# Kernel tuning notes

Measured on AMD Instinct MI355X. Metric: run time of the kernel, lower is better.

Reference implementation:

```python
import jax, jax.numpy as jnp
import numpy as np

NUM_HEADS = 12


def setup_inputs() -> dict:
    key = jax.random.key(0)
    ks = jax.random.split(key, 7)
    B, H, W, C = 1, 64, 64, 768
    hd = C // NUM_HEADS
    return {
        "x": jax.random.normal(ks[0], (B, H, W, C), dtype=jnp.float32),
        "qkv_w": jax.random.normal(ks[1], (C, 3 * C), dtype=jnp.float32) * 0.02,
        "qkv_b": jax.random.normal(ks[2], (3 * C,), dtype=jnp.float32) * 0.02,
        "proj_w": jax.random.normal(ks[3], (C, C), dtype=jnp.float32) * 0.02,
        "proj_b": jax.random.normal(ks[4], (C,), dtype=jnp.float32) * 0.02,
        "rel_pos_h": jax.random.normal(ks[5], (2 * H - 1, hd), dtype=jnp.float32) * 0.02,
        "rel_pos_w": jax.random.normal(ks[6], (2 * W - 1, hd), dtype=jnp.float32) * 0.02,
    }


def _rel_table(size, rel_pos):
    # q_size == k_size so relative_coords = i - j + (size - 1)
    coords = jnp.arange(size)[:, None] - jnp.arange(size)[None, :] + (size - 1)
    return rel_pos[coords]  # [size, size, head_dim]


def reference(x, qkv_w, qkv_b, proj_w, proj_b, rel_pos_h, rel_pos_w):
    B, H, W, C = x.shape
    nh = NUM_HEADS
    hd = C // nh
    scale = hd ** -0.5
    N = H * W

    qkv = x.reshape(B, N, C) @ qkv_w + qkv_b  # [B, N, 3C]
    qkv = qkv.reshape(B, N, 3, nh, hd).transpose(2, 0, 3, 1, 4).reshape(3, B * nh, N, hd)
    q, k, v = qkv[0], qkv[1], qkv[2]

    attn = jnp.einsum("bqd,bkd->bqk", q * scale, k)  # [B*nh, N, N]

    # decomposed relative position bias
    Rh = _rel_table(H, rel_pos_h)  # [H, H, hd]
    Rw = _rel_table(W, rel_pos_w)  # [W, W, hd]
    qr = q.reshape(B * nh, H, W, hd)
    rel_h = jnp.einsum("bhwc,hkc->bhwk", qr, Rh)  # [B*nh, H, W, H]
    rel_w = jnp.einsum("bhwc,wkc->bhwk", qr, Rw)  # [B*nh, H, W, W]
    bias = rel_h[..., :, None] + rel_w[..., None, :]  # [B*nh, H, W, H, W]
    attn = attn + bias.reshape(B * nh, N, N)

    attn = jax.nn.softmax(attn, axis=-1)
    out = jnp.einsum("bqk,bkd->bqd", attn, v)  # [B*nh, N, hd]
    out = out.reshape(B, nh, H, W, hd).transpose(0, 2, 3, 1, 4).reshape(B, H, W, C)
    return out @ proj_w + proj_b
```

## Files before the change

kernel.cpp:

```cpp
#include <hip/hip_runtime.h>
#include <math.h>

#define NHEADS 12
#define NTOK 4096
#define LOG2E 1.44269504f

typedef __attribute__((ext_vector_type(8))) short bf8v;
typedef __attribute__((ext_vector_type(4))) float f4v;
typedef __attribute__((ext_vector_type(16))) float f16v;

__device__ __forceinline__ unsigned short f2bf(float f) {
  unsigned int u = __float_as_uint(f);
  u += 0x7fffu + ((u >> 16) & 1u);
  return (unsigned short)(u >> 16);
}
__device__ __forceinline__ bf8v pack8(float4 a, float4 b) {
  bf8v v;
  v[0] = (short)f2bf(a.x); v[1] = (short)f2bf(a.y);
  v[2] = (short)f2bf(a.z); v[3] = (short)f2bf(a.w);
  v[4] = (short)f2bf(b.x); v[5] = (short)f2bf(b.y);
  v[6] = (short)f2bf(b.z); v[7] = (short)f2bf(b.w);
  return v;
}
__device__ __forceinline__ unsigned pkbf(float hi, float lo) {
  return __builtin_amdgcn_perm(__float_as_uint(hi) + 0x8000u,
                               __float_as_uint(lo) + 0x8000u, 0x07060302u);
}
__device__ __forceinline__ void gload_lds16(const void* g, void* l) {
  __builtin_amdgcn_global_load_lds(
      (const __attribute__((address_space(1))) void*)g,
      (__attribute__((address_space(3))) void*)l, 16, 0, 0);
}

__device__ __forceinline__ void tcvt_body(
    const float* __restrict__ in, short* __restrict__ out, int R, int C,
    int bx, int by, int t, float (*Ts)[65])
{
    const int bc = bx * 64, br = by * 64;
    {
        const int r = t >> 2, c0 = (t & 3) * 16;
        const float* src = in + (size_t)(br + r) * C + bc + c0;
#pragma unroll
        for (int i = 0; i < 4; ++i) {
            float4 a = *(const float4*)(src + 4 * i);
            Ts[r][c0 + 4 * i + 0] = a.x;
            Ts[r][c0 + 4 * i + 1] = a.y;
            Ts[r][c0 + 4 * i + 2] = a.z;
            Ts[r][c0 + 4 * i + 3] = a.w;
        }
    }
    __syncthreads();
    const int c = t >> 2, r0 = (t & 3) * 16;
    short* dst = out + (size_t)(bc + c) * R + br + r0;
#pragma unroll
    for (int p = 0; p < 2; ++p) {
        bf8v v;
#pragma unroll
        for (int i = 0; i < 8; ++i) v[i] = (short)f2bf(Ts[r0 + p * 8 + i][c]);
        *(bf8v*)(dst + p * 8) = v;
    }
}

__global__ __launch_bounds__(256) void prep_kernel(
    const float* __restrict__ x, const float* __restrict__ qkvw,
    const float* __restrict__ pw, short* __restrict__ xh,
    short* __restrict__ wqkvT, short* __restrict__ pwT)
{
    __shared__ float Ts[64][65];
    const int bid = blockIdx.x, t = threadIdx.x;
    if (bid < 1536) {
        const size_t i = ((size_t)bid * 256 + t) * 8;
        float4 a = *(const float4*)(x + i);
        float4 b = *(const float4*)(x + i + 4);
        *(bf8v*)(xh + i) = pack8(a, b);
    } else if (bid < 1968) {
        const int idx = bid - 1536;
        tcvt_body(qkvw, wqkvT, 768, 2304, idx % 36, idx / 36, t, Ts);
    } else {
        const int idx = bid - 1968;
        tcvt_body(pw, pwT, 768, 768, idx % 12, idx / 12, t, Ts);
    }
}

__global__ __launch_bounds__(256) void qkv_mfma_kernel(
    const short* __restrict__ xh, const short* __restrict__ wT,
    const float* __restrict__ bias, short* __restrict__ qbh,
    short* __restrict__ kbh, short* __restrict__ vbT)
{
    __shared__ __align__(16) short As[128 * 32];
    __shared__ __align__(16) short Bs[96 * 32];
    const int t = threadIdx.x;
    const int w = t >> 6, lane = t & 63;
    const int l15 = lane & 15, l4 = lane >> 4;
    const int wr = w >> 1, wc = w & 1;
    const int row0 = blockIdx.y * 128, col0 = blockIdx.x * 96;
    const int ldr = lane >> 2;
    const int ldk = (lane & 3) * 8;

    f4v acc[4][3] = {};
    const short* aBase = xh + (size_t)(row0 + w * 32 + ldr) * 768 + ldk;
    const short* bBase0 = wT + (size_t)(col0 + w * 16 + ldr) * 768 + ldk;
    const short* bBase1 = wT + (size_t)(col0 + 64 + w * 16 + ldr) * 768 + ldk;

    for (int kk = 0; kk < 768; kk += 32) {
        __syncthreads();
#pragma unroll
        for (int c = 0; c < 2; ++c)
            gload_lds16(aBase + (size_t)c * 16 * 768 + kk,
                        &As[(w * 32 + c * 16) * 32]);
        gload_lds16(bBase0 + kk, &Bs[(w * 16) * 32]);
        if (w < 2)
            gload_lds16(bBase1 + kk, &Bs[(64 + w * 16) * 32]);
        __syncthreads();
        bf8v af[4], bg[3];
#pragma unroll
        for (int i = 0; i < 4; ++i)
            af[i] = *(const bf8v*)&As[(wr * 64 + 16 * i + l15) * 32 + l4 * 8];
#pragma unroll
        for (int j = 0; j < 3; ++j)
            bg[j] = *(const bf8v*)&Bs[(wc * 48 + 16 * j + l15) * 32 + l4 * 8];
#pragma unroll
        for (int i = 0; i < 4; ++i)
#pragma unroll
            for (int j = 0; j < 3; ++j)
                acc[i][j] = __builtin_amdgcn_mfma_f32_16x16x32_bf16(
                    af[i], bg[j], acc[i][j], 0, 0, 0);
    }

#pragma unroll
    for (int j = 0; j < 3; ++j) {
        const int n = col0 + wc * 48 + 16 * j + l15;
        const int s = n / 768;
        const int rm = n - s * 768;
        const int h = rm >> 6, d = rm & 63;
        const float bv = bias[n];
        if (s == 2) {
            short* vdst = vbT + (size_t)(h * 64 + d) * NTOK;
#pragma unroll
            for (int i = 0; i < 4; ++i) {
                const int m = row0 + wr * 64 + 16 * i + l4 * 4;
                short4 pv;
                pv.x = (short)f2bf(acc[i][j][0] + bv);
                pv.y = (short)f2bf(acc[i][j][1] + bv);
                pv.z = (short)f2bf(acc[i][j][2] + bv);
                pv.w = (short)f2bf(acc[i][j][3] + bv);
                *(short4*)(vdst + m) = pv;
            }
        } else {
            short* dst = (s == 0) ? qbh : kbh;
#pragma unroll
            for (int i = 0; i < 4; ++i) {
                const int m = row0 + wr * 64 + 16 * i + l4 * 4;
#pragma unroll
                for (int r = 0; r < 4; ++r)
                    dst[((size_t)h * NTOK + m + r) * 64 + d] =
                        (short)f2bf(acc[i][j][r] + bv);
            }
        }
    }
}

union FlashSMem {
    struct {
        short Ks[128][68];
        short Vt[64][132];
        float relHs[64][65];
    };
    float U[128 * 65];
    struct {
        float OEp[64][64];
        float lEp[64];
    };
};

__global__ __launch_bounds__(256, 3) void flash_mfma_kernel(
    const short* __restrict__ qbh, const short* __restrict__ kbh,
    const short* __restrict__ vbT, const float* __restrict__ rpw,
    const float* __restrict__ rph, short* __restrict__ aob)
{
    __shared__ __align__(16) FlashSMem sm;

    const int t = threadIdx.x;
    const int qt = blockIdx.x, head = blockIdx.y;
    const int row0 = qt * 64;
    const int lane = t & 63, w = t >> 6;
    const int qh2 = w & 1, th = w >> 1;
    const int l31 = lane & 31, hf = lane >> 5;
    const size_t hB = (size_t)head * NTOK * 64;
    const float SC = 0.125f * LOG2E;

    const int q = row0 + qh2 * 32 + l31;
    bf8v bQ[4];
    {
        const short* qsrc = qbh + hB + (size_t)q * 64;
#pragma unroll
        for (int ks = 0; ks < 4; ++ks)
            bQ[ks] = *(const bf8v*)(qsrc + ks * 16 + hf * 8);
    }
    const int sx = t >> 2;
    const int sck = (t & 3) * 16;
    const int scv = (t & 3) * 32;
    const short* kptr = kbh + hB + (size_t)sx * 64 + sck;
    const short* vptr = vbT + ((size_t)head * 64 + sx) * NTOK + scv;
    bf8v kpf[4], vpf[4];
    kpf[0] = *(const bf8v*)(kptr);
    kpf[1] = *(const bf8v*)(kptr + 8);
    kpf[2] = *(const bf8v*)(kptr + 64 * 64);
    kpf[3] = *(const bf8v*)(kptr + 64 * 64 + 8);
    vpf[0] = *(const bf8v*)(vptr);
    vpf[1] = *(const bf8v*)(vptr + 8);
    vpf[2] = *(const bf8v*)(vptr + 16);
    vpf[3] = *(const bf8v*)(vptr + 24);

#pragma unroll
    for (int jt2 = 0; jt2 < 2; ++jt2) {
        const int jt = 2 * th + jt2;
        int j = jt * 32 + l31;
        if (j > 126) j = 0;
        const float* asrc = rpw + (size_t)j * 64;
        f16v c = {};
#pragma unroll
        for (int ks = 0; ks < 4; ++ks) {
            float4 u0 = *(const float4*)(asrc + ks * 16 + hf * 8);
            float4 u1 = *(const float4*)(asrc + ks * 16 + hf * 8 + 4);
            c = __builtin_amdgcn_mfma_f32_32x32x16_bf16(
                pack8(u0, u1), bQ[ks], c, 0, 0, 0);
        }
#pragma unroll
        for (int reg = 0; reg < 16; ++reg)
            sm.U[(jt * 32 + (reg & 3) + 8 * (reg >> 2) + 4 * hf) * 65 +
                 qh2 * 32 + l31] = c[reg];
    }
    __syncthreads();
    const int qw = qh2 * 32 + l31;
    uint2 rwp[2][4];
#pragma unroll
    for (int t32 = 0; t32 < 2; ++t32)
#pragma unroll
        for (int g = 0; g < 4; ++g) {
            const int kw = t32 * 32 + 8 * g + 4 * hf;
            const float v0 = sm.U[(qw + 63 - kw) * 65 + qw] * LOG2E;
            const float v1 = sm.U[(qw + 62 - kw) * 65 + qw] * LOG2E;
            const float v2 = sm.U[(qw + 61 - kw) * 65 + qw] * LOG2E;
            const float v3 = sm.U[(qw + 60 - kw) * 65 + qw] * LOG2E;
            rwp[t32][g].x = pkbf(v1, v0);
            rwp[t32][g].y = pkbf(v3, v2);
        }
    __syncthreads();

    {
        const int kh = th * 32 + l31;
        const float* asrc = rph + (size_t)(qt + 63 - kh) * 64;
        f16v c = {};
#pragma unroll
        for (int ks = 0; ks < 4; ++ks) {
            float4 u0 = *(const float4*)(asrc + ks * 16 + hf * 8);
            float4 u1 = *(const float4*)(asrc + ks * 16 + hf * 8 + 4);
            u0.x *= LOG2E; u0.y *= LOG2E; u0.z *= LOG2E; u0.w *= LOG2E;
            u1.x *= LOG2E; u1.y *= LOG2E; u1.z *= LOG2E; u1.w *= LOG2E;
            c = __builtin_amdgcn_mfma_f32_32x32x16_bf16(
                pack8(u0, u1), bQ[ks], c, 0, 0, 0);
        }
#pragma unroll
        for (int reg = 0; reg < 16; ++reg)
            sm.relHs[th * 32 + (reg & 3) + 8 * (reg >> 2) + 4 * hf]
                    [qh2 * 32 + l31] = c[reg];
    }

    f16v O[2] = {{}, {}};
    float lsum = 0.f;

    for (int it = 0; it < 32; ++it) {
        __syncthreads();
        *(bf8v*)&sm.Ks[sx][sck] = kpf[0];
        *(bf8v*)&sm.Ks[sx][sck + 8] = kpf[1];
        *(bf8v*)&sm.Ks[sx + 64][sck] = kpf[2];
        *(bf8v*)&sm.Ks[sx + 64][sck + 8] = kpf[3];
        *(bf8v*)&sm.Vt[sx][scv] = vpf[0];
        *(bf8v*)&sm.Vt[sx][scv + 8] = vpf[1];
        *(bf8v*)&sm.Vt[sx][scv + 16] = vpf[2];
        *(bf8v*)&sm.Vt[sx][scv + 24] = vpf[3];
        {
            const int itn = (it < 31) ? it + 1 : 31;
            const short* kp = kptr + (size_t)itn * 128 * 64;
            const short* vp = vptr + itn * 128;
            kpf[0] = *(const bf8v*)kp;
            kpf[1] = *(const bf8v*)(kp + 8);
            kpf[2] = *(const bf8v*)(kp + 64 * 64);
            kpf[3] = *(const bf8v*)(kp + 64 * 64 + 8);
            vpf[0] = *(const bf8v*)vp;
            vpf[1] = *(const bf8v*)(vp + 8);
            vpf[2] = *(const bf8v*)(vp + 16);
            vpf[3] = *(const bf8v*)(vp + 24);
        }
        __syncthreads();

        f16v acc[2] = {{}, {}};
#pragma unroll
        for (int ks = 0; ks < 4; ++ks)
#pragma unroll
            for (int t32 = 0; t32 < 2; ++t32)
                acc[t32] = __builtin_amdgcn_mfma_f32_32x32x16_bf16(
                    *(const bf8v*)&sm.Ks[th * 64 + t32 * 32 + l31]
                                        [ks * 16 + hf * 8],
                    bQ[ks], acc[t32], 0, 0, 0);

        const float rh = sm.relHs[2 * it + th][qh2 * 32 + l31];

        unsigned xg[2][4], yg[2][4];
#pragma unroll
        for (int t32 = 0; t32 < 2; ++t32) {
            float sub = 0.f;
#pragma unroll
            for (int g = 0; g < 4; ++g) {
                const unsigned u0 = rwp[t32][g].x;
                const unsigned u1 = rwp[t32][g].y;
                const float b0 = __uint_as_float(u0 << 16) + rh;
                const float b1 = __uint_as_float(u0 & 0xffff0000u) + rh;
                const float b2 = __uint_as_float(u1 << 16) + rh;
                const float b3 = __uint_as_float(u1 & 0xffff0000u) + rh;
                const float e0 = __builtin_amdgcn_exp2f(
                    fmaf(acc[t32][4 * g + 0], SC, b0));
                const float e1 = __builtin_amdgcn_exp2f(
                    fmaf(acc[t32][4 * g + 1], SC, b1));
                const float e2 = __builtin_amdgcn_exp2f(
                    fmaf(acc[t32][4 * g + 2], SC, b2));
                const float e3 = __builtin_amdgcn_exp2f(
                    fmaf(acc[t32][4 * g + 3], SC, b3));
                sub += (e0 + e1) + (e2 + e3);
                xg[t32][g] = pkbf(e1, e0);
                yg[t32][g] = pkbf(e3, e2);
            }
            lsum += sub;
        }

#pragma unroll
        for (int t32 = 0; t32 < 2; ++t32)
#pragma unroll
            for (int ks2 = 0; ks2 < 2; ++ks2) {
                auto px = __builtin_amdgcn_permlane32_swap(
                    xg[t32][2 * ks2], xg[t32][2 * ks2 + 1], false, false);
                auto py = __builtin_amdgcn_permlane32_swap(
                    yg[t32][2 * ks2], yg[t32][2 * ks2 + 1], false, false);
                int4 av;
                av.x = (int)px[0];
                av.y = (int)py[0];
                av.z = (int)px[1];
                av.w = (int)py[1];
                union { int4 i; bf8v v; } u; u.i = av;
#pragma unroll
                for (int nt = 0; nt < 2; ++nt)
                    O[nt] = __builtin_amdgcn_mfma_f32_32x32x16_bf16(
                        u.v,
                        *(const bf8v*)&sm.Vt[nt * 32 + l31]
                                            [th * 64 + t32 * 32 + ks2 * 16 +
                                             hf * 8],
                        O[nt], 0, 0, 0);
            }
    }

    lsum += __shfl_xor(lsum, 32);
    __syncthreads();
    if (th == 1) {
#pragma unroll
        for (int nt = 0; nt < 2; ++nt)
#pragma unroll
            for (int reg = 0; reg < 16; ++reg) {
                const int qr = (reg & 3) + 8 * (reg >> 2) + 4 * hf;
                sm.OEp[qh2 * 32 + qr][nt * 32 + l31] = O[nt][reg];
            }
        if (lane < 32) sm.lEp[qh2 * 32 + l31] = lsum;
    }
    __syncthreads();
    if (th == 0) {
        lsum += sm.lEp[qh2 * 32 + l31];
        const float linv = 1.0f / lsum;
#pragma unroll
        for (int nt = 0; nt < 2; ++nt)
#pragma unroll
            for (int reg = 0; reg < 16; ++reg) {
                const int qr = (reg & 3) + 8 * (reg >> 2) + 4 * hf;
                const float li = __shfl(linv, qr);
                const float o =
                    O[nt][reg] + sm.OEp[qh2 * 32 + qr][nt * 32 + l31];
                aob[(size_t)(row0 + qh2 * 32 + qr) * 768 + head * 64 +
                    nt * 32 + l31] = (short)f2bf(o * li);
            }
    }
}

__global__ __launch_bounds__(256) void proj_mfma_kernel(
    const short* __restrict__ aoh, const short* __restrict__ pwT,
    const float* __restrict__ bias, float* __restrict__ out)
{
    __shared__ __align__(16) short As[64 * 32];
    __shared__ __align__(16) short Bs[128 * 32];
    const int t = threadIdx.x;
    const int w = t >> 6, lane = t & 63;
    const int l15 = lane & 15, l4 = lane >> 4;
    const int wr = w >> 1, wc = w & 1;
    const int row0 = blockIdx.y * 64, col0 = blockIdx.x * 128;
    const int ldr = lane >> 2;
    const int ldk = (lane & 3) * 8;

    f4v acc[2][4] = {};
    const short* aBase = aoh + (size_t)(row0 + w * 16 + ldr) * 768 + ldk;
    const short* bBase = pwT + (size_t)(col0 + w * 32 + ldr) * 768 + ldk;

    for (int kk = 0; kk < 768; kk += 32) {
        __syncthreads();
        gload_lds16(aBase + kk, &As[(w * 16) * 32]);
#pragma unroll
        for (int c = 0; c < 2; ++c)
            gload_lds16(bBase + (size_t)c * 16 * 768 + kk,
                        &Bs[(w * 32 + c * 16) * 32]);
        __syncthreads();
        bf8v af[2], bg[4];
#pragma unroll
        for (int i = 0; i < 2; ++i)
            af[i] = *(const bf8v*)&As[(wr * 32 + 16 * i + l15) * 32 + l4 * 8];
#pragma unroll
        for (int j = 0; j < 4; ++j)
            bg[j] = *(const bf8v*)&Bs[(wc * 64 + 16 * j + l15) * 32 + l4 * 8];
#pragma unroll
        for (int i = 0; i < 2; ++i)
#pragma unroll
            for (int j = 0; j < 4; ++j)
                acc[i][j] = __builtin_amdgcn_mfma_f32_16x16x32_bf16(
                    af[i], bg[j], acc[i][j], 0, 0, 0);
    }

#pragma unroll
    for (int j = 0; j < 4; ++j) {
        const int n = col0 + wc * 64 + 16 * j + l15;
        const float bv = bias[n];
#pragma unroll
        for (int i = 0; i < 2; ++i) {
            const int m = row0 + wr * 32 + 16 * i + l4 * 4;
#pragma unroll
            for (int r = 0; r < 4; ++r)
                out[(size_t)(m + r) * 768 + n] = acc[i][j][r] + bv;
        }
    }
}

extern "C" void kernel_launch(void* const* d_in, const int* in_sizes, int n_in,
                              void* d_out, int out_size, void* d_ws,
                              size_t ws_size, hipStream_t stream)
{
    (void)in_sizes; (void)n_in; (void)out_size; (void)ws_size;
    const float* x    = (const float*)d_in[0];
    const float* qkvw = (const float*)d_in[1];
    const float* qkvb = (const float*)d_in[2];
    const float* pw   = (const float*)d_in[3];
    const float* pb   = (const float*)d_in[4];
    const float* rph  = (const float*)d_in[5];
    const float* rpw  = (const float*)d_in[6];
    float* out = (float*)d_out;

    const size_t S = (size_t)NHEADS * NTOK * 64;
    short* qbh  = (short*)d_ws;
    short* kbh  = qbh + S;
    short* vbT  = kbh + S;
    short* xh   = vbT + S;
    short* aob  = xh;
    short* wqkvT = xh + S;
    short* pwT  = wqkvT + (size_t)2304 * 768;

    prep_kernel<<<dim3(2112), 256, 0, stream>>>(x, qkvw, pw, xh, wqkvT, pwT);
    qkv_mfma_kernel<<<dim3(24, 32), 256, 0, stream>>>(xh, wqkvT, qkvb,
                                                      qbh, kbh, vbT);
    flash_mfma_kernel<<<dim3(64, NHEADS), 256, 0, stream>>>(qbh, kbh, vbT,
                                                            rpw, rph, aob);
    proj_mfma_kernel<<<dim3(6, 64), 256, 0, stream>>>(aob, pwT, pb, out);
}
```

Before: 222.0 us.

## Load K/V directly from global into registers, drop LDS staging and key split

The flash attention kernel now uses 128-thread blocks of two waves. Each wave loops over all 64 key tiles of 64 keys. It reads K and V fragments straight from global memory into registers and prefetches the next K tile, instead of staging K/Vt through shared memory with two barriers per iteration. The key-dimension split across waves and the cross-wave LDS reduction of O and the softmax sum are removed. This cuts LDS traffic and synchronisation, but each wave now fetches its own K/V copy (more global/L2 traffic), V loads are not prefetched, and per-block parallelism is halved.

```diff
diff --git a/kernel.cpp b/kernel.cpp
--- a/kernel.cpp
+++ b/kernel.cpp
@@ -161,19 +161,11 @@
 }
 
 union FlashSMem {
-    struct {
-        short Ks[128][68];
-        short Vt[64][132];
-        float relHs[64][65];
-    };
-    float U[128 * 65];
-    struct {
-        float OEp[64][64];
-        float lEp[64];
-    };
+    float U[128][66];
+    float relHs[64][66];
 };
 
-__global__ __launch_bounds__(256, 3) void flash_mfma_kernel(
+__global__ __launch_bounds__(128, 2) void flash_mfma_kernel(
     const short* __restrict__ qbh, const short* __restrict__ kbh,
     const short* __restrict__ vbT, const float* __restrict__ rpw,
     const float* __restrict__ rph, short* __restrict__ aob)
@@ -183,8 +175,7 @@
     const int t = threadIdx.x;
     const int qt = blockIdx.x, head = blockIdx.y;
     const int row0 = qt * 64;
-    const int lane = t & 63, w = t >> 6;
-    const int qh2 = w & 1, th = w >> 1;
+    const int lane = t & 63, qh2 = t >> 6;
     const int l31 = lane & 31, hf = lane >> 5;
     const size_t hB = (size_t)head * NTOK * 64;
     const float SC = 0.125f * LOG2E;
@@ -197,24 +188,9 @@
         for (int ks = 0; ks < 4; ++ks)
             bQ[ks] = *(const bf8v*)(qsrc + ks * 16 + hf * 8);
     }
-    const int sx = t >> 2;
-    const int sck = (t & 3) * 16;
-    const int scv = (t & 3) * 32;
-    const short* kptr = kbh + hB + (size_t)sx * 64 + sck;
-    const short* vptr = vbT + ((size_t)head * 64 + sx) * NTOK + scv;
-    bf8v kpf[4], vpf[4];
-    kpf[0] = *(const bf8v*)(kptr);
-    kpf[1] = *(const bf8v*)(kptr + 8);
-    kpf[2] = *(const bf8v*)(kptr + 64 * 64);
-    kpf[3] = *(const bf8v*)(kptr + 64 * 64 + 8);
-    vpf[0] = *(const bf8v*)(vptr);
-    vpf[1] = *(const bf8v*)(vptr + 8);
-    vpf[2] = *(const bf8v*)(vptr + 16);
-    vpf[3] = *(const bf8v*)(vptr + 24);
-
-#pragma unroll
-    for (int jt2 = 0; jt2 < 2; ++jt2) {
-        const int jt = 2 * th + jt2;
+
+#pragma unroll
+    for (int jt = 0; jt < 4; ++jt) {
         int j = jt * 32 + l31;
         if (j > 126) j = 0;
         const float* asrc = rpw + (size_t)j * 64;
@@ -228,8 +204,8 @@
         }
 #pragma unroll
         for (int reg = 0; reg < 16; ++reg)
-            sm.U[(jt * 32 + (reg & 3) + 8 * (reg >> 2) + 4 * hf) * 65 +
-                 qh2 * 32 + l31] = c[reg];
+            sm.U[jt * 32 + (reg & 3) + 8 * (reg >> 2) + 4 * hf]
+                [qh2 * 32 + l31] = c[reg];
     }
     __syncthreads();
     const int qw = qh2 * 32 + l31;
@@ -239,17 +215,18 @@
 #pragma unroll
         for (int g = 0; g < 4; ++g) {
             const int kw = t32 * 32 + 8 * g + 4 * hf;
-            const float v0 = sm.U[(qw + 63 - kw) * 65 + qw] * LOG2E;
-            const float v1 = sm.U[(qw + 62 - kw) * 65 + qw] * LOG2E;
-            const float v2 = sm.U[(qw + 61 - kw) * 65 + qw] * LOG2E;
-            const float v3 = sm.U[(qw + 60 - kw) * 65 + qw] * LOG2E;
+            const float v0 = sm.U[qw + 63 - kw][qw] * LOG2E;
+            const float v1 = sm.U[qw + 62 - kw][qw] * LOG2E;
+            const float v2 = sm.U[qw + 61 - kw][qw] * LOG2E;
+            const float v3 = sm.U[qw + 60 - kw][qw] * LOG2E;
             rwp[t32][g].x = pkbf(v1, v0);
             rwp[t32][g].y = pkbf(v3, v2);
         }
     __syncthreads();
 
-    {
-        const int kh = th * 32 + l31;
+#pragma unroll
+    for (int kt = 0; kt < 2; ++kt) {
+        const int kh = kt * 32 + l31;
         const float* asrc = rph + (size_t)(qt + 63 - kh) * 64;
         f16v c = {};
 #pragma unroll
@@ -263,37 +240,36 @@
         }
 #pragma unroll
         for (int reg = 0; reg < 16; ++reg)
-            sm.relHs[th * 32 + (reg & 3) + 8 * (reg >> 2) + 4 * hf]
+            sm.relHs[kt * 32 + (reg & 3) + 8 * (reg >> 2) + 4 * hf]
                     [qh2 * 32 + l31] = c[reg];
     }
+    __syncthreads();
+
+    const short* kbase = kbh + hB + (size_t)l31 * 64 + hf * 8;
+    const short* vbase = vbT + ((size_t)head * 64 + l31) * NTOK + hf * 8;
+
+    bf8v kA[2][4];
+#pragma unroll
+    for (int t32 = 0; t32 < 2; ++t32)
+#pragma unroll
+        for (int ks = 0; ks < 4; ++ks)
+            kA[t32][ks] = *(const bf8v*)(kbase + (size_t)(t32 * 32) * 64 +
+                                         ks * 16);
 
     f16v O[2] = {{}, {}};
     float lsum = 0.f;
 
-    for (int it = 0; it < 32; ++it) {
-        __syncthreads();
-        *(bf8v*)&sm.Ks[sx][sck] = kpf[0];
-        *(bf8v*)&sm.Ks[sx][sck + 8] = kpf[1];
-        *(bf8v*)&sm.Ks[sx + 64][sck] = kpf[2];
-        *(bf8v*)&sm.Ks[sx + 64][sck + 8] = kpf[3];
-        *(bf8v*)&sm.Vt[sx][scv] = vpf[0];
-        *(bf8v*)&sm.Vt[sx][scv + 8] = vpf[1];
-        *(bf8v*)&sm.Vt[sx][scv + 16] = vpf[2];
-        *(bf8v*)&sm.Vt[sx][scv + 24] = vpf[3];
-        {
-            const int itn = (it < 31) ? it + 1 : 31;
-            const short* kp = kptr + (size_t)itn * 128 * 64;
-            const short* vp = vptr + itn * 128;
-            kpf[0] = *(const bf8v*)kp;
-            kpf[1] = *(const bf8v*)(kp + 8);
-            kpf[2] = *(const bf8v*)(kp + 64 * 64);
-            kpf[3] = *(const bf8v*)(kp + 64 * 64 + 8);
-            vpf[0] = *(const bf8v*)vp;
-            vpf[1] = *(const bf8v*)(vp + 8);
-            vpf[2] = *(const bf8v*)(vp + 16);
-            vpf[3] = *(const bf8v*)(vp + 24);
-        }
-        __syncthreads();
+    for (int it = 0; it < 64; ++it) {
+        bf8v vB[2][2][2];
+#pragma unroll
+        for (int nt = 0; nt < 2; ++nt)
+#pragma unroll
+            for (int t32 = 0; t32 < 2; ++t32)
+#pragma unroll
+                for (int ks2 = 0; ks2 < 2; ++ks2)
+                    vB[t32][ks2][nt] = *(const bf8v*)(
+                        vbase + (size_t)nt * 32 * NTOK + it * 64 + t32 * 32 +
+                        ks2 * 16);
 
         f16v acc[2] = {{}, {}};
 #pragma unroll
@@ -301,11 +277,20 @@
 #pragma unroll
             for (int t32 = 0; t32 < 2; ++t32)
                 acc[t32] = __builtin_amdgcn_mfma_f32_32x32x16_bf16(
-                    *(const bf8v*)&sm.Ks[th * 64 + t32 * 32 + l31]
-                                        [ks * 16 + hf * 8],
-                    bQ[ks], acc[t32], 0, 0, 0);
-
-        const float rh = sm.relHs[2 * it + th][qh2 * 32 + l31];
+                    kA[t32][ks], bQ[ks], acc[t32], 0, 0, 0);
+
+        bf8v kN[2][4];
+        {
+            const int itn = (it < 63) ? it + 1 : 63;
+#pragma unroll
+            for (int t32 = 0; t32 < 2; ++t32)
+#pragma unroll
+                for (int ks = 0; ks < 4; ++ks)
+                    kN[t32][ks] = *(const bf8v*)(
+                        kbase + (size_t)(itn * 64 + t32 * 32) * 64 + ks * 16);
+        }
+
+        const float rh = sm.relHs[it][qh2 * 32 + l31];
 
         unsigned xg[2][4], yg[2][4];
 #pragma unroll
@@ -351,42 +336,27 @@
 #pragma unroll
                 for (int nt = 0; nt < 2; ++nt)
                     O[nt] = __builtin_amdgcn_mfma_f32_32x32x16_bf16(
-                        u.v,
-                        *(const bf8v*)&sm.Vt[nt * 32 + l31]
-                                            [th * 64 + t32 * 32 + ks2 * 16 +
-                                             hf * 8],
-                        O[nt], 0, 0, 0);
+                        u.v, vB[t32][ks2][nt], O[nt], 0, 0, 0);
             }
+
+#pragma unroll
+        for (int t32 = 0; t32 < 2; ++t32)
+#pragma unroll
+            for (int ks = 0; ks < 4; ++ks)
+                kA[t32][ks] = kN[t32][ks];
     }
 
     lsum += __shfl_xor(lsum, 32);
-    __syncthreads();
-    if (th == 1) {
-#pragma unroll
-        for (int nt = 0; nt < 2; ++nt)
-#pragma unroll
-            for (int reg = 0; reg < 16; ++reg) {
-                const int qr = (reg & 3) + 8 * (reg >> 2) + 4 * hf;
-                sm.OEp[qh2 * 32 + qr][nt * 32 + l31] = O[nt][reg];
-            }
-        if (lane < 32) sm.lEp[qh2 * 32 + l31] = lsum;
-    }
-    __syncthreads();
-    if (th == 0) {
-        lsum += sm.lEp[qh2 * 32 + l31];
-        const float linv = 1.0f / lsum;
-#pragma unroll
-        for (int nt = 0; nt < 2; ++nt)
-#pragma unroll
-            for (int reg = 0; reg < 16; ++reg) {
-                const int qr = (reg & 3) + 8 * (reg >> 2) + 4 * hf;
-                const float li = __shfl(linv, qr);
-                const float o =
-                    O[nt][reg] + sm.OEp[qh2 * 32 + qr][nt * 32 + l31];
-                aob[(size_t)(row0 + qh2 * 32 + qr) * 768 + head * 64 +
-                    nt * 32 + l31] = (short)f2bf(o * li);
-            }
-    }
+    const float linv = 1.0f / lsum;
+#pragma unroll
+    for (int nt = 0; nt < 2; ++nt)
+#pragma unroll
+        for (int reg = 0; reg < 16; ++reg) {
+            const int qr = (reg & 3) + 8 * (reg >> 2) + 4 * hf;
+            const float li = __shfl(linv, qr);
+            aob[(size_t)(row0 + qh2 * 32 + qr) * 768 + head * 64 + nt * 32 +
+                l31] = (short)f2bf(O[nt][reg] * li);
+        }
 }
 
 __global__ __launch_bounds__(256) void proj_mfma_kernel(
@@ -470,7 +440,7 @@
     prep_kernel<<<dim3(2112), 256, 0, stream>>>(x, qkvw, pw, xh, wqkvT, pwT);
     qkv_mfma_kernel<<<dim3(24, 32), 256, 0, stream>>>(xh, wqkvT, qkvb,
                                                       qbh, kbh, vbT);
-    flash_mfma_kernel<<<dim3(64, NHEADS), 256, 0, stream>>>(qbh, kbh, vbT,
+    flash_mfma_kernel<<<dim3(64, NHEADS), 128, 0, stream>>>(qbh, kbh, vbT,
                                                             rpw, rph, aob);
     proj_mfma_kernel<<<dim3(6, 64), 256, 0, stream>>>(aob, pwT, pb, out);
 }
```

Measured after the change: 312.6 us. 1.41x slower.
